# Kernel optimization log

Hardware: AMD Instinct MI355X
Metric: run time of the kernel (lower is better)

Reference implementation:

```python
import jax, jax.numpy as jnp
import numpy as np

DIM = 1024
HEADS = 16
DIM_HEAD = DIM // HEADS  # 64


def setup_inputs() -> dict:
    key = jax.random.key(0)
    k1, k2, k3 = jax.random.split(key, 3)
    x = jax.random.normal(k1, (4, 2048, DIM), dtype=jnp.float32)
    # Linear weights stored as [in, out] so y = x @ W (torch Linear uses x @ W.T; init is random either way)
    w_qkv = jax.random.normal(k2, (DIM, 3 * DIM), dtype=jnp.float32) * (DIM ** -0.5)
    w_out = jax.random.normal(k3, (DIM, DIM), dtype=jnp.float32) * (DIM ** -0.5)
    return {"x": x, "w_qkv": w_qkv, "w_out": w_out}


def reference(x, w_qkv, w_out):
    b, t, d = x.shape
    h, dh = HEADS, DIM_HEAD
    qkv = x @ w_qkv  # [b, t, 3*h*dh]
    q, k, v = jnp.split(qkv, 3, axis=-1)
    split_heads = lambda a: a.reshape(b, t, h, dh).transpose(0, 2, 1, 3)  # [b,h,t,dh]
    q, k, v = map(split_heads, (q, k, v))
    # NOTE: original scales by full model dim d, not per-head dim
    scale = d ** (-0.5)
    dots = jnp.einsum('bhie,bhje->bhij', q, k) * scale  # [b,h,t,t]
    attn = jax.nn.softmax(dots, axis=-1)
    out = jnp.einsum('bhij,bhje->bhie', attn, v)  # [b,h,t,dh]
    out = out.transpose(0, 2, 1, 3).reshape(b, t, h * dh)
    return out @ w_out
```

## Files before the change

kernel.cpp:

```cpp
#include <hip/hip_runtime.h>


typedef __bf16 bf16x8 __attribute__((ext_vector_type(8)));
typedef __bf16 bf16x4 __attribute__((ext_vector_type(4)));
typedef __bf16 bf16x2 __attribute__((ext_vector_type(2)));
typedef float f32x4 __attribute__((ext_vector_type(4)));
typedef float f32x2 __attribute__((ext_vector_type(2)));
typedef float f32x16 __attribute__((ext_vector_type(16)));
typedef unsigned short ushort8 __attribute__((ext_vector_type(8)));

#define MFMA16(a, b, c) __builtin_amdgcn_mfma_f32_16x16x32_bf16((a), (b), (c), 0, 0, 0)
#define MFMA32(a, b, c) __builtin_amdgcn_mfma_f32_32x32x16_bf16((a), (b), (c), 0, 0, 0)

__device__ __forceinline__ unsigned short f2bf(float f) {
  unsigned int u = __float_as_uint(f);
  u = (u + 0x7FFFu + ((u >> 16) & 1u)) >> 16;
  return (unsigned short)u;
}

__device__ __forceinline__ float fast_exp2(float x) {
#if __has_builtin(__builtin_amdgcn_exp2f)
  return __builtin_amdgcn_exp2f(x);
#else
  float r;
  asm("v_exp_f32 %0, %1" : "=v"(r) : "v"(x));
  return r;
#endif
}

__device__ __forceinline__ void gload_lds16(const unsigned short* g, unsigned short* l) {
  __builtin_amdgcn_global_load_lds(
      (const __attribute__((address_space(1))) unsigned int*)g,
      (__attribute__((address_space(3))) unsigned int*)l, 16, 0, 0);
}

__device__ __forceinline__ void half_swap(unsigned int a, unsigned int b,
                                          unsigned int& x, unsigned int& y,
                                          bool H) {
#if __has_builtin(__builtin_amdgcn_permlane32_swap)
  auto r = __builtin_amdgcn_permlane32_swap(a, b, false, false);
  x = (unsigned int)r[0];
  y = (unsigned int)r[1];
#else
  unsigned int oa = (unsigned int)__shfl_xor((int)a, 32);
  unsigned int ob = (unsigned int)__shfl_xor((int)b, 32);
  x = H ? ob : a;
  y = H ? b : oa;
#endif
}

__global__ __launch_bounds__(256) void prep_kernel(
    const float* __restrict__ x, unsigned short* __restrict__ xb,
    const float* __restrict__ wqkv, unsigned short* __restrict__ WqkvT,
    const float* __restrict__ wout, unsigned short* __restrict__ WoutT) {
  const int bid = blockIdx.x;
  const int tid = threadIdx.x;
  if (bid < 4096) {
    int i = (bid * 256 + tid) * 8;
    float4 a = *(const float4*)&x[i];
    float4 b = *(const float4*)&x[i + 4];
    ushort8 o = {f2bf(a.x), f2bf(a.y), f2bf(a.z), f2bf(a.w),
                 f2bf(b.x), f2bf(b.y), f2bf(b.z), f2bf(b.w)};
    *(ushort8*)&xb[i] = o;
    return;
  }
  __shared__ float t[32][33];
  const float* in;
  unsigned short* out;
  int C, scale_limit, c0, r0;
  if (bid < 4096 + 3072) {
    int tj = bid - 4096;
    in = wqkv; out = WqkvT; C = 3072; scale_limit = 1024;
    c0 = (tj % 96) * 32; r0 = (tj / 96) * 32;
  } else {
    int tj = bid - 7168;
    in = wout; out = WoutT; C = 1024; scale_limit = 0;
    c0 = (tj & 31) * 32; r0 = (tj >> 5) * 32;
  }
  const float kQScale = 0.045084220027780106f;
#pragma unroll
  for (int i = 0; i < 4; ++i) {
    int e = tid + i * 256;
    int r = e >> 5, c = e & 31;
    t[r][c] = in[(size_t)(r0 + r) * C + c0 + c];
  }
  __syncthreads();
#pragma unroll
  for (int i = 0; i < 4; ++i) {
    int e = tid + i * 256;
    int r = e >> 5, c = e & 31;
    float v = t[c][r];
    if (c0 + r < scale_limit) v *= kQScale;
    out[(size_t)(c0 + r) * 1024 + r0 + c] = f2bf(v);
  }
}

template <int MODE>
__global__ __launch_bounds__(256) void gemm_bt(
    const unsigned short* __restrict__ A, const unsigned short* __restrict__ Bt,
    void* __restrict__ Cv, unsigned short* __restrict__ VT,
    int M, int N, int K) {
  __shared__ unsigned short As[128 * 32];
  __shared__ unsigned short Bs[128 * 32];
  const int tid = threadIdx.x;
  const int wave = tid >> 6, lane = tid & 63;
  const int g = lane >> 4, ln = lane & 15;
  const int wm = wave >> 1, wn = wave & 1;
  const long bm = (long)blockIdx.y * 128;
  const long bn = (long)blockIdx.x * 128;

  f32x4 acc[4][4];
#pragma unroll
  for (int i = 0; i < 4; ++i)
#pragma unroll
    for (int j = 0; j < 4; ++j) acc[i][j] = (f32x4){0.f, 0.f, 0.f, 0.f};

  const int srow = wave * 32 + (lane >> 2);
  const int scol = (lane & 3) * 8;
  const unsigned short* gA0 = A + (bm + srow) * (long)K + scol;
  const unsigned short* gA1 = gA0 + 16 * (long)K;
  const unsigned short* gB0 = Bt + (bn + srow) * (long)K + scol;
  const unsigned short* gB1 = gB0 + 16 * (long)K;
  unsigned short* lA0 = &As[wave * 1024];
  unsigned short* lA1 = &As[wave * 1024 + 512];
  unsigned short* lB0 = &Bs[wave * 1024];
  unsigned short* lB1 = &Bs[wave * 1024 + 512];

  for (int k0 = 0; k0 < K; k0 += 32) {
    __syncthreads();
    gload_lds16(gA0 + k0, lA0);
    gload_lds16(gA1 + k0, lA1);
    gload_lds16(gB0 + k0, lB0);
    gload_lds16(gB1 + k0, lB1);
    __syncthreads();

    bf16x8 af[4], bfr[4];
#pragma unroll
    for (int i = 0; i < 4; ++i) {
      af[i]  = *(const bf16x8*)&As[(wm * 64 + i * 16 + ln) * 32 + g * 8];
      bfr[i] = *(const bf16x8*)&Bs[(wn * 64 + i * 16 + ln) * 32 + g * 8];
    }
    __builtin_amdgcn_s_setprio(1);
#pragma unroll
    for (int i = 0; i < 4; ++i)
#pragma unroll
      for (int j = 0; j < 4; ++j)
        acc[i][j] = MFMA16(af[i], bfr[j], acc[i][j]);
    __builtin_amdgcn_s_setprio(0);
  }

  const long crow = bm + wm * 64, ccol = bn + wn * 64;
  if (MODE == 2 && bn >= 2048) {
#pragma unroll
    for (int i = 0; i < 4; ++i)
#pragma unroll
      for (int j = 0; j < 4; ++j) {
        int nv = (int)(ccol + j * 16 + ln) - 2048;
        int h = nv >> 6, dh = nv & 63;
        long tg = crow + i * 16 + g * 4;
        int b = (int)(tg >> 11), tl = (int)(tg & 2047);
        size_t idx = (size_t)(b * 16 + h) * 131072 + (size_t)dh * 2048 + tl;
        bf16x4 o = {(__bf16)acc[i][j][0], (__bf16)acc[i][j][1],
                    (__bf16)acc[i][j][2], (__bf16)acc[i][j][3]};
        *(bf16x4*)&VT[idx] = o;
      }
  } else {
#pragma unroll
    for (int i = 0; i < 4; ++i)
#pragma unroll
      for (int j = 0; j < 4; ++j)
#pragma unroll
        for (int r = 0; r < 4; ++r) {
          long idx = (crow + i * 16 + g * 4 + r) * (long)N + ccol + j * 16 + ln;
          if (MODE == 1)
            ((float*)Cv)[idx] = acc[i][j][r];
          else
            ((unsigned short*)Cv)[idx] = f2bf(acc[i][j][r]);
        }
  }
}

__global__ __launch_bounds__(256, 2) void attn_kernel(
    const unsigned short* __restrict__ qkv, const unsigned short* __restrict__ VT,
    unsigned short* __restrict__ attn_out) {
  __shared__ unsigned short Ks[2][64][64];
  __shared__ unsigned short Vs[2][64][64];

  const int tid = threadIdx.x;
  const int wave = tid >> 6, lane = tid & 63;
  const int l31 = lane & 31, hb = lane >> 5;

  const int wg = (blockIdx.x & 7) * 64 + (blockIdx.x >> 3);
  const int bh = wg >> 3, qc = wg & 7;
  const int b = bh >> 4, head = bh & 15;
  const int q0 = qc * 256 + wave * 64;

  bf16x8 qfA[4], qfB[4];
  {
    size_t baseA = (size_t)(b * 2048 + q0 + l31) * 3072 + head * 64 + 8 * hb;
    size_t baseB = baseA + (size_t)32 * 3072;
    qfA[0] = *(const bf16x8*)&qkv[baseA];
    qfA[1] = *(const bf16x8*)&qkv[baseA + 16];
    qfA[2] = *(const bf16x8*)&qkv[baseA + 32];
    qfA[3] = *(const bf16x8*)&qkv[baseA + 48];
    qfB[0] = *(const bf16x8*)&qkv[baseB];
    qfB[1] = *(const bf16x8*)&qkv[baseB + 16];
    qfB[2] = *(const bf16x8*)&qkv[baseB + 32];
    qfB[3] = *(const bf16x8*)&qkv[baseB + 48];
  }

  f32x16 oaccA[2], oaccB[2];
#pragma unroll
  for (int i = 0; i < 16; ++i) {
    oaccA[0][i] = 0.f; oaccA[1][i] = 0.f;
    oaccB[0][i] = 0.f; oaccB[1][i] = 0.f;
  }
  f32x2 lsA = {0.f, 0.f}, lsB = {0.f, 0.f};

  const int srow = tid >> 3;
  const int sc = tid & 7;
  const int swz = (sc ^ (srow & 7)) * 8;
  const unsigned short* gK =
      qkv + (size_t)b * 2048 * 3072 + 1024 + head * 64 + (size_t)srow * 3072 + swz;
  const unsigned short* gV = VT + (size_t)bh * 131072 + (size_t)srow * 2048 + swz;
  const int wrow = wave * 8;

  auto STAGE = [&](int buf, int j) {
    gload_lds16(gK + (size_t)j * 3072,        &Ks[buf][wrow][0]);
    gload_lds16(gK + (size_t)(j + 32) * 3072, &Ks[buf][wrow + 32][0]);
    gload_lds16(gV + j,                       &Vs[buf][wrow][0]);
    gload_lds16(gV + 32 * 2048 + j,           &Vs[buf][wrow + 32][0]);
  };

  const int myx = l31 & 7;
  const bool H = (hb != 0);

  STAGE(0, 0);
  asm volatile("s_waitcnt vmcnt(0)" ::: "memory");
  __syncthreads();

  int cur = 0;
  for (int j0 = 0; j0 < 2048; j0 += 64) {
    if (j0 + 64 < 2048) STAGE(cur ^ 1, j0 + 64);

#pragma unroll
    for (int kt = 0; kt < 2; ++kt) {
      f32x16 saA, saB;
#pragma unroll
      for (int i = 0; i < 16; ++i) { saA[i] = 0.f; saB[i] = 0.f; }
      __builtin_amdgcn_s_setprio(1);
#pragma unroll
      for (int t = 0; t < 4; ++t) {
        bf16x8 kf = *(const bf16x8*)&Ks[cur][kt * 32 + l31][((2 * t + hb) ^ myx) * 8];
        saA = MFMA32(kf, qfA[t], saA);
        saB = MFMA32(kf, qfB[t], saB);
      }
      __builtin_amdgcn_s_setprio(0);

      unsigned int pkwA[8], pkwB[8];
#pragma unroll
      for (int j = 0; j < 8; ++j) {
        float a0 = fast_exp2(saA[2 * j]);
        float a1 = fast_exp2(saA[2 * j + 1]);
        lsA += (f32x2){a0, a1};
        bf16x2 av = {(__bf16)a0, (__bf16)a1};
        pkwA[j] = __builtin_bit_cast(unsigned int, av);
        float b0 = fast_exp2(saB[2 * j]);
        float b1 = fast_exp2(saB[2 * j + 1]);
        lsB += (f32x2){b0, b1};
        bf16x2 bv = {(__bf16)b0, (__bf16)b1};
        pkwB[j] = __builtin_bit_cast(unsigned int, bv);
      }

      union { unsigned int u[4]; bf16x8 v; } pfA0, pfA1, pfB0, pfB1;
      half_swap(pkwA[0], pkwA[2], pfA0.u[0], pfA0.u[2], H);
      half_swap(pkwA[1], pkwA[3], pfA0.u[1], pfA0.u[3], H);
      half_swap(pkwA[4], pkwA[6], pfA1.u[0], pfA1.u[2], H);
      half_swap(pkwA[5], pkwA[7], pfA1.u[1], pfA1.u[3], H);
      half_swap(pkwB[0], pkwB[2], pfB0.u[0], pfB0.u[2], H);
      half_swap(pkwB[1], pkwB[3], pfB0.u[1], pfB0.u[3], H);
      half_swap(pkwB[4], pkwB[6], pfB1.u[0], pfB1.u[2], H);
      half_swap(pkwB[5], pkwB[7], pfB1.u[1], pfB1.u[3], H);

      __builtin_amdgcn_s_setprio(1);
#pragma unroll
      for (int mt = 0; mt < 2; ++mt) {
        bf16x8 vf0 = *(const bf16x8*)&Vs[cur][mt * 32 + l31][((4 * kt + hb) ^ myx) * 8];
        bf16x8 vf1 = *(const bf16x8*)&Vs[cur][mt * 32 + l31][((4 * kt + 2 + hb) ^ myx) * 8];
        oaccA[mt] = MFMA32(vf0, pfA0.v, oaccA[mt]);
        oaccA[mt] = MFMA32(vf1, pfA1.v, oaccA[mt]);
        oaccB[mt] = MFMA32(vf0, pfB0.v, oaccB[mt]);
        oaccB[mt] = MFMA32(vf1, pfB1.v, oaccB[mt]);
      }
      __builtin_amdgcn_s_setprio(0);
    }

    asm volatile("s_waitcnt vmcnt(0)" ::: "memory");
    __syncthreads();
    cur ^= 1;
  }

  {
    float l = lsA.x + lsA.y;
    l += __shfl_xor(l, 32);
    float inv = 1.0f / l;
    size_t row = (size_t)(b * 2048 + q0 + l31) * 1024 + head * 64;
#pragma unroll
    for (int mt = 0; mt < 2; ++mt)
#pragma unroll
      for (int rq = 0; rq < 4; ++rq) {
        bf16x4 o = {(__bf16)(oaccA[mt][4 * rq + 0] * inv),
                    (__bf16)(oaccA[mt][4 * rq + 1] * inv),
                    (__bf16)(oaccA[mt][4 * rq + 2] * inv),
                    (__bf16)(oaccA[mt][4 * rq + 3] * inv)};
        *(bf16x4*)&attn_out[row + mt * 32 + 8 * rq + 4 * hb] = o;
      }
  }
  {
    float l = lsB.x + lsB.y;
    l += __shfl_xor(l, 32);
    float inv = 1.0f / l;
    size_t row = (size_t)(b * 2048 + q0 + 32 + l31) * 1024 + head * 64;
#pragma unroll
    for (int mt = 0; mt < 2; ++mt)
#pragma unroll
      for (int rq = 0; rq < 4; ++rq) {
        bf16x4 o = {(__bf16)(oaccB[mt][4 * rq + 0] * inv),
                    (__bf16)(oaccB[mt][4 * rq + 1] * inv),
                    (__bf16)(oaccB[mt][4 * rq + 2] * inv),
                    (__bf16)(oaccB[mt][4 * rq + 3] * inv)};
        *(bf16x4*)&attn_out[row + mt * 32 + 8 * rq + 4 * hb] = o;
      }
  }
}

extern "C" void kernel_launch(void* const* d_in, const int* in_sizes, int n_in,
                              void* d_out, int out_size, void* d_ws, size_t ws_size,
                              hipStream_t stream) {
  (void)in_sizes; (void)n_in; (void)out_size; (void)ws_size;
  const float* x_f     = (const float*)d_in[0];
  const float* w_qkv_f = (const float*)d_in[1];
  const float* w_out_f = (const float*)d_in[2];
  float* out = (float*)d_out;

  char* ws = (char*)d_ws;
  unsigned short* qkv   = (unsigned short*)(ws);
  unsigned short* attn  = (unsigned short*)(ws + 50331648);
  unsigned short* VT    = (unsigned short*)(ws + 67108864);
  unsigned short* WqkvT = (unsigned short*)(ws + 83886080);
  unsigned short* WoutT = (unsigned short*)(ws + 90177536);
  unsigned short* xb    = (unsigned short*)(ws + 92274688);

  prep_kernel<<<8192, 256, 0, stream>>>(x_f, xb, w_qkv_f, WqkvT, w_out_f, WoutT);
  gemm_bt<2><<<dim3(24, 64), 256, 0, stream>>>(xb, WqkvT, qkv, VT, 8192, 3072, 1024);
  attn_kernel<<<512, 256, 0, stream>>>(qkv, VT, attn);
  gemm_bt<1><<<dim3(8, 64), 256, 0, stream>>>(attn, WoutT, out, nullptr, 8192, 1024, 1024);
}
```

Before: 184.2 us.

## Drop LDS staging in attention; load K/V straight to registers per wave

The attention kernel now runs one wave per block (2048 blocks of 64 threads) and loads K and V fragments directly from global memory into registers, with K double-buffered in registers. The shared-memory staging, swizzling and __syncthreads barriers are gone. The aim is to remove LDS traffic and barrier stalls. In exchange, each wave re-reads K/V from global memory, which quadruples global/L2 traffic, and register pressure goes up.

```diff
diff --git a/kernel.cpp b/kernel.cpp
--- a/kernel.cpp
+++ b/kernel.cpp
@@ -180,20 +180,86 @@
   }
 }
 
-__global__ __launch_bounds__(256, 2) void attn_kernel(
+#define PREF_K(KB, J)                                            \
+  {                                                              \
+    const unsigned short* kp = gKbase + (size_t)(J) * 3072;      \
+    KB[0] = *(const bf16x8*)&kp[0];                              \
+    KB[1] = *(const bf16x8*)&kp[16];                             \
+    KB[2] = *(const bf16x8*)&kp[32];                             \
+    KB[3] = *(const bf16x8*)&kp[48];                             \
+    const unsigned short* kq = kp + 32 * 3072;                   \
+    KB[4] = *(const bf16x8*)&kq[0];                              \
+    KB[5] = *(const bf16x8*)&kq[16];                             \
+    KB[6] = *(const bf16x8*)&kq[32];                             \
+    KB[7] = *(const bf16x8*)&kq[48];                             \
+  }
+
+#define LOAD_V(VB, J)                                            \
+  {                                                              \
+    const unsigned short* vp = gVbase + (J);                     \
+    VB[0] = *(const bf16x8*)&vp[0];                              \
+    VB[1] = *(const bf16x8*)&vp[16];                             \
+    VB[2] = *(const bf16x8*)&vp[32];                             \
+    VB[3] = *(const bf16x8*)&vp[48];                             \
+    const unsigned short* vq = vp + 32 * 2048;                   \
+    VB[4] = *(const bf16x8*)&vq[0];                              \
+    VB[5] = *(const bf16x8*)&vq[16];                             \
+    VB[6] = *(const bf16x8*)&vq[32];                             \
+    VB[7] = *(const bf16x8*)&vq[48];                             \
+  }
+
+#define ATTN_TILE(KB, VB)                                                     \
+  _Pragma("unroll") for (int kt = 0; kt < 2; ++kt) {                          \
+    f32x16 saA, saB;                                                          \
+    _Pragma("unroll") for (int i = 0; i < 16; ++i) { saA[i] = 0.f; saB[i] = 0.f; } \
+    __builtin_amdgcn_s_setprio(1);                                            \
+    _Pragma("unroll") for (int t = 0; t < 4; ++t) {                           \
+      saA = MFMA32(KB[kt * 4 + t], qfA[t], saA);                              \
+      saB = MFMA32(KB[kt * 4 + t], qfB[t], saB);                              \
+    }                                                                         \
+    __builtin_amdgcn_s_setprio(0);                                            \
+    unsigned int pkwA[8], pkwB[8];                                            \
+    _Pragma("unroll") for (int j = 0; j < 8; ++j) {                           \
+      float a0 = fast_exp2(saA[2 * j]);                                       \
+      float a1 = fast_exp2(saA[2 * j + 1]);                                   \
+      lsA += (f32x2){a0, a1};                                                 \
+      bf16x2 av = {(__bf16)a0, (__bf16)a1};                                   \
+      pkwA[j] = __builtin_bit_cast(unsigned int, av);                         \
+      float b0 = fast_exp2(saB[2 * j]);                                       \
+      float b1 = fast_exp2(saB[2 * j + 1]);                                   \
+      lsB += (f32x2){b0, b1};                                                 \
+      bf16x2 bv = {(__bf16)b0, (__bf16)b1};                                   \
+      pkwB[j] = __builtin_bit_cast(unsigned int, bv);                         \
+    }                                                                         \
+    union Up { unsigned int u[4]; bf16x8 v; } pfA0, pfA1, pfB0, pfB1;         \
+    half_swap(pkwA[0], pkwA[2], pfA0.u[0], pfA0.u[2], H);                     \
+    half_swap(pkwA[1], pkwA[3], pfA0.u[1], pfA0.u[3], H);                     \
+    half_swap(pkwA[4], pkwA[6], pfA1.u[0], pfA1.u[2], H);                     \
+    half_swap(pkwA[5], pkwA[7], pfA1.u[1], pfA1.u[3], H);                     \
+    half_swap(pkwB[0], pkwB[2], pfB0.u[0], pfB0.u[2], H);                     \
+    half_swap(pkwB[1], pkwB[3], pfB0.u[1], pfB0.u[3], H);                     \
+    half_swap(pkwB[4], pkwB[6], pfB1.u[0], pfB1.u[2], H);                     \
+    half_swap(pkwB[5], pkwB[7], pfB1.u[1], pfB1.u[3], H);                     \
+    __builtin_amdgcn_s_setprio(1);                                            \
+    _Pragma("unroll") for (int mt = 0; mt < 2; ++mt) {                        \
+      oaccA[mt] = MFMA32(VB[mt * 4 + kt * 2 + 0], pfA0.v, oaccA[mt]);         \
+      oaccA[mt] = MFMA32(VB[mt * 4 + kt * 2 + 1], pfA1.v, oaccA[mt]);         \
+      oaccB[mt] = MFMA32(VB[mt * 4 + kt * 2 + 0], pfB0.v, oaccB[mt]);         \
+      oaccB[mt] = MFMA32(VB[mt * 4 + kt * 2 + 1], pfB1.v, oaccB[mt]);         \
+    }                                                                         \
+    __builtin_amdgcn_s_setprio(0);                                            \
+  }
+
+__global__ __launch_bounds__(64, 2) void attn_kernel(
     const unsigned short* __restrict__ qkv, const unsigned short* __restrict__ VT,
     unsigned short* __restrict__ attn_out) {
-  __shared__ unsigned short Ks[2][64][64];
-  __shared__ unsigned short Vs[2][64][64];
-
   const int tid = threadIdx.x;
-  const int wave = tid >> 6, lane = tid & 63;
-  const int l31 = lane & 31, hb = lane >> 5;
-
-  const int wg = (blockIdx.x & 7) * 64 + (blockIdx.x >> 3);
-  const int bh = wg >> 3, qc = wg & 7;
+  const int l31 = tid & 31, hb = tid >> 5;
+
+  const int wg = (blockIdx.x & 7) * 256 + (blockIdx.x >> 3);
+  const int bh = wg >> 5, qw = wg & 31;
   const int b = bh >> 4, head = bh & 15;
-  const int q0 = qc * 256 + wave * 64;
+  const int q0 = qw * 64;
 
   bf16x8 qfA[4], qfB[4];
   {
@@ -216,88 +282,29 @@
     oaccB[0][i] = 0.f; oaccB[1][i] = 0.f;
   }
   f32x2 lsA = {0.f, 0.f}, lsB = {0.f, 0.f};
-
-  const int srow = tid >> 3;
-  const int sc = tid & 7;
-  const int swz = (sc ^ (srow & 7)) * 8;
-  const unsigned short* gK =
-      qkv + (size_t)b * 2048 * 3072 + 1024 + head * 64 + (size_t)srow * 3072 + swz;
-  const unsigned short* gV = VT + (size_t)bh * 131072 + (size_t)srow * 2048 + swz;
-  const int wrow = wave * 8;
-
-  auto STAGE = [&](int buf, int j) {
-    gload_lds16(gK + (size_t)j * 3072,        &Ks[buf][wrow][0]);
-    gload_lds16(gK + (size_t)(j + 32) * 3072, &Ks[buf][wrow + 32][0]);
-    gload_lds16(gV + j,                       &Vs[buf][wrow][0]);
-    gload_lds16(gV + 32 * 2048 + j,           &Vs[buf][wrow + 32][0]);
-  };
-
-  const int myx = l31 & 7;
   const bool H = (hb != 0);
 
-  STAGE(0, 0);
-  asm volatile("s_waitcnt vmcnt(0)" ::: "memory");
-  __syncthreads();
-
-  int cur = 0;
-  for (int j0 = 0; j0 < 2048; j0 += 64) {
-    if (j0 + 64 < 2048) STAGE(cur ^ 1, j0 + 64);
-
-#pragma unroll
-    for (int kt = 0; kt < 2; ++kt) {
-      f32x16 saA, saB;
-#pragma unroll
-      for (int i = 0; i < 16; ++i) { saA[i] = 0.f; saB[i] = 0.f; }
-      __builtin_amdgcn_s_setprio(1);
-#pragma unroll
-      for (int t = 0; t < 4; ++t) {
-        bf16x8 kf = *(const bf16x8*)&Ks[cur][kt * 32 + l31][((2 * t + hb) ^ myx) * 8];
-        saA = MFMA32(kf, qfA[t], saA);
-        saB = MFMA32(kf, qfB[t], saB);
-      }
-      __builtin_amdgcn_s_setprio(0);
-
-      unsigned int pkwA[8], pkwB[8];
-#pragma unroll
-      for (int j = 0; j < 8; ++j) {
-        float a0 = fast_exp2(saA[2 * j]);
-        float a1 = fast_exp2(saA[2 * j + 1]);
-        lsA += (f32x2){a0, a1};
-        bf16x2 av = {(__bf16)a0, (__bf16)a1};
-        pkwA[j] = __builtin_bit_cast(unsigned int, av);
-        float b0 = fast_exp2(saB[2 * j]);
-        float b1 = fast_exp2(saB[2 * j + 1]);
-        lsB += (f32x2){b0, b1};
-        bf16x2 bv = {(__bf16)b0, (__bf16)b1};
-        pkwB[j] = __builtin_bit_cast(unsigned int, bv);
-      }
-
-      union { unsigned int u[4]; bf16x8 v; } pfA0, pfA1, pfB0, pfB1;
-      half_swap(pkwA[0], pkwA[2], pfA0.u[0], pfA0.u[2], H);
-      half_swap(pkwA[1], pkwA[3], pfA0.u[1], pfA0.u[3], H);
-      half_swap(pkwA[4], pkwA[6], pfA1.u[0], pfA1.u[2], H);
-      half_swap(pkwA[5], pkwA[7], pfA1.u[1], pfA1.u[3], H);
-      half_swap(pkwB[0], pkwB[2], pfB0.u[0], pfB0.u[2], H);
-      half_swap(pkwB[1], pkwB[3], pfB0.u[1], pfB0.u[3], H);
-      half_swap(pkwB[4], pkwB[6], pfB1.u[0], pfB1.u[2], H);
-      half_swap(pkwB[5], pkwB[7], pfB1.u[1], pfB1.u[3], H);
-
-      __builtin_amdgcn_s_setprio(1);
-#pragma unroll
-      for (int mt = 0; mt < 2; ++mt) {
-        bf16x8 vf0 = *(const bf16x8*)&Vs[cur][mt * 32 + l31][((4 * kt + hb) ^ myx) * 8];
-        bf16x8 vf1 = *(const bf16x8*)&Vs[cur][mt * 32 + l31][((4 * kt + 2 + hb) ^ myx) * 8];
-        oaccA[mt] = MFMA32(vf0, pfA0.v, oaccA[mt]);
-        oaccA[mt] = MFMA32(vf1, pfA1.v, oaccA[mt]);
-        oaccB[mt] = MFMA32(vf0, pfB0.v, oaccB[mt]);
-        oaccB[mt] = MFMA32(vf1, pfB1.v, oaccB[mt]);
-      }
-      __builtin_amdgcn_s_setprio(0);
+  const unsigned short* gKbase =
+      qkv + (size_t)b * 6291456 + 1024 + head * 64 + (size_t)l31 * 3072 + 8 * hb;
+  const unsigned short* gVbase =
+      VT + (size_t)bh * 131072 + (size_t)l31 * 2048 + 8 * hb;
+
+  bf16x8 kE[8], kO[8];
+  PREF_K(kE, 0);
+
+  for (int j0 = 0; j0 < 2048; j0 += 128) {
+    {
+      bf16x8 vb[8];
+      LOAD_V(vb, j0);
+      PREF_K(kO, j0 + 64);
+      ATTN_TILE(kE, vb);
     }
-
-    asm volatile("s_waitcnt vmcnt(0)" ::: "memory");
-    __syncthreads();
-    cur ^= 1;
+    {
+      bf16x8 vb[8];
+      LOAD_V(vb, j0 + 64);
+      if (j0 + 128 < 2048) PREF_K(kE, j0 + 128);
+      ATTN_TILE(kO, vb);
+    }
   }
 
   {
@@ -353,6 +360,6 @@
 
   prep_kernel<<<8192, 256, 0, stream>>>(x_f, xb, w_qkv_f, WqkvT, w_out_f, WoutT);
   gemm_bt<2><<<dim3(24, 64), 256, 0, stream>>>(xb, WqkvT, qkv, VT, 8192, 3072, 1024);
-  attn_kernel<<<512, 256, 0, stream>>>(qkv, VT, attn);
+  attn_kernel<<<2048, 64, 0, stream>>>(qkv, VT, attn);
   gemm_bt<1><<<dim3(8, 64), 256, 0, stream>>>(attn, WoutT, out, nullptr, 8192, 1024, 1024);
 }
```

After: 254.9 us. 38.3% more time.
